# Performance work log

Hardware: AMD Instinct MI355X
Metric: run time of the kernel (lower is better)

Reference implementation:

```python
import jax, jax.numpy as jnp
import numpy as np

N = 50000      # nodes
E = 800000     # edges (avg degree 16)
F_IN = 128     # num_features
H = 64         # hidden_dim
G = 64         # graphs in batch


def setup_inputs() -> dict:
    key = jax.random.key(0)
    ks = jax.random.split(key, 20)
    inp = {
        "x": jax.random.normal(ks[0], (N, F_IN), jnp.float32),
        "edge_index": jax.random.randint(ks[1], (2, E), 0, N, dtype=jnp.int32).astype(jnp.int64),
        "batch": jnp.sort(jax.random.randint(ks[2], (N,), 0, G, dtype=jnp.int32)).astype(jnp.int64),
    }
    # GraphConv layer dims: in -> out
    dims = [(F_IN, H), (H, 2 * H), (2 * H, 3 * H), (3 * H, H)]
    k = 3
    for i, (din, dout) in enumerate(dims):
        s = 1.0 / np.sqrt(din).astype(np.float32)
        inp[f"w{i+1}_rel"] = jax.random.normal(ks[k], (din, dout), jnp.float32) * s
        inp[f"w{i+1}_root"] = jax.random.normal(ks[k + 1], (din, dout), jnp.float32) * s
        inp[f"b{i+1}"] = jnp.zeros((dout,), jnp.float32)
        k += 2
    inp["head_w"] = jax.random.normal(ks[k], (H, 1), jnp.float32) * (1.0 / np.sqrt(H).astype(np.float32))
    inp["head_b"] = jnp.zeros((1,), jnp.float32)
    return inp


def _graph_conv(x, src, dst, w_rel, w_root, b):
    # PyG GraphConv: out = lin_rel(sum_{j in N(i)} x_j) + lin_root(x_i)
    agg = jax.ops.segment_sum(x[src], dst, num_segments=N)  # [N, din]
    return agg @ w_rel + b + x @ w_root


def reference(x, edge_index, batch,
              w1_rel, w1_root, b1,
              w2_rel, w2_root, b2,
              w3_rel, w3_root, b3,
              w4_rel, w4_root, b4,
              head_w, head_b):
    src, dst = edge_index[0], edge_index[1]
    h = jax.nn.relu(_graph_conv(x, src, dst, w1_rel, w1_root, b1))
    h = jax.nn.relu(_graph_conv(h, src, dst, w2_rel, w2_root, b2))
    h = jax.nn.relu(_graph_conv(h, src, dst, w3_rel, w3_root, b3))
    h = _graph_conv(h, src, dst, w4_rel, w4_root, b4)          # [N, H]
    # global_mean_pool over graph ids
    sums = jax.ops.segment_sum(h, batch, num_segments=G)       # [G, H]
    counts = jax.ops.segment_sum(jnp.ones((N,), h.dtype), batch, num_segments=G)
    pooled = sums / jnp.maximum(counts, 1.0)[:, None]          # [G, H]
    return pooled @ head_w + head_b                            # [G, 1]
```

## Files before the change

### kernel.cpp

```cpp
#include <hip/hip_runtime.h>


#define NNODES 50000
#define NEDGES 800000
#define NGRAPH 64
#define NBUK 256
#define BSZ 196
#define EPB (NEDGES / NBUK)
#define CVT_NB (NNODES * 128 / 4 / 256)
#define PACK_NB (160 * 512 / 256)
#define RGRID ((NNODES + 127) / 128)
#define RCHUNK ((RGRID + 7) / 8)

typedef __attribute__((ext_vector_type(8))) __bf16 bf16x8;
typedef __attribute__((ext_vector_type(16))) float f32x16;

__device__ __forceinline__ unsigned short f2bf(float f) {
    unsigned u = __float_as_uint(f);
    u += 0x7fff + ((u >> 16) & 1);
    return (unsigned short)(u >> 16);
}
__device__ __forceinline__ float bf2f(unsigned b) {
    return __uint_as_float(b << 16);
}

__device__ __forceinline__ void dma16(const void* g, void* l) {
    __builtin_amdgcn_global_load_lds(
        (const __attribute__((address_space(1))) void*)g,
        (__attribute__((address_space(3))) void*)l, 16, 0, 0);
}


__global__ void hist_kernel(const int* __restrict__ dst, int* __restrict__ cnt) {
    __shared__ int h[NBUK];
    int tid = threadIdx.x, k = blockIdx.x;
    h[tid] = 0;
    __syncthreads();
    int end = (k + 1) * EPB;
    for (int i = k * EPB + tid; i < end; i += 256)
        atomicAdd(&h[dst[i] / BSZ], 1);
    __syncthreads();
    cnt[tid * NBUK + k] = h[tid];
}

__global__ void scan1_kernel(int* __restrict__ a, int* __restrict__ bsum, int n) {
    __shared__ int buf[256];
    int tid = threadIdx.x;
    int i = blockIdx.x * 256 + tid;
    int v = (i < n) ? a[i] : 0;
    buf[tid] = v;
    __syncthreads();
    #pragma unroll
    for (int off = 1; off < 256; off <<= 1) {
        int t = (tid >= off) ? buf[tid - off] : 0;
        __syncthreads();
        buf[tid] += t;
        __syncthreads();
    }
    if (i < n) a[i] = buf[tid] - v;
    if (tid == 255) bsum[blockIdx.x] = buf[255];
}

__global__ void scan2_kernel(int* __restrict__ bsum, int nb) {
    __shared__ int buf[256];
    int tid = threadIdx.x;
    int v = (tid < nb) ? bsum[tid] : 0;
    buf[tid] = v;
    __syncthreads();
    #pragma unroll
    for (int off = 1; off < 256; off <<= 1) {
        int t = (tid >= off) ? buf[tid - off] : 0;
        __syncthreads();
        buf[tid] += t;
        __syncthreads();
    }
    if (tid < nb) bsum[tid] = buf[tid] - v;
}

__global__ void partition_kernel(const int* __restrict__ src, const int* __restrict__ dst,
                                 const int* __restrict__ cnt, const int* __restrict__ bsum,
                                 unsigned long long* __restrict__ pedge) {
    __shared__ int lbase[NBUK];
    int tid = threadIdx.x, k = blockIdx.x;
    lbase[tid] = cnt[tid * NBUK + k] + bsum[tid];
    __syncthreads();
    int end = (k + 1) * EPB;
    for (int i = k * EPB + tid; i < end; i += 256) {
        int s = src[i], d = dst[i];
        int pos = atomicAdd(&lbase[d / BSZ], 1);
        pedge[pos] = (unsigned long long)(unsigned)s | ((unsigned long long)(unsigned)d << 32);
    }
}

__global__ void build_kernel(const unsigned long long* __restrict__ pedge,
                             const int* __restrict__ bsum,
                             int* __restrict__ rp, int* __restrict__ csr) {
    __shared__ int sdeg[256], sc[256], sbase[256], sfill[256];
    int tid = threadIdx.x, b = blockIdx.x;
    int node0 = b * BSZ;
    int ncnt = NNODES - node0;
    if (ncnt > BSZ) ncnt = BSZ;
    if (ncnt < 0) ncnt = 0;
    int seg0 = bsum[b];
    int seg1 = (b + 1 < NBUK) ? bsum[b + 1] : NEDGES;
    sdeg[tid] = 0;
    sfill[tid] = 0;
    __syncthreads();
    for (int i = seg0 + tid; i < seg1; i += 256)
        atomicAdd(&sdeg[(int)(pedge[i] >> 32) - node0], 1);
    __syncthreads();
    sc[tid] = sdeg[tid];
    __syncthreads();
    #pragma unroll
    for (int off = 1; off < 256; off <<= 1) {
        int t = (tid >= off) ? sc[tid - off] : 0;
        __syncthreads();
        sc[tid] += t;
        __syncthreads();
    }
    sbase[tid] = sc[tid] - sdeg[tid];
    if (tid < ncnt) rp[node0 + tid] = seg0 + sbase[tid];
    if (b == NBUK - 1 && tid == 0) rp[NNODES] = NEDGES;
    __syncthreads();
    for (int i = seg0 + tid; i < seg1; i += 256) {
        unsigned long long p = pedge[i];
        int d = (int)(p >> 32) - node0;
        int pos = atomicAdd(&sfill[d], 1);
        csr[seg0 + sbase[d] + pos] = (int)(p & 0xffffffffu);
    }
}


__device__ __forceinline__ void pack32(const float* __restrict__ W, unsigned short* __restrict__ dst,
                                       int KS_tot, int ks0, int dcols, int ct0,
                                       int tl, int ksl, int lane, int j) {
    int k = ksl * 16 + ((lane >> 5) << 3) + j;
    int col = tl * 32 + (lane & 31);
    dst[(((size_t)(ct0 + tl) * KS_tot + (ks0 + ksl)) * 64 + lane) * 8 + j] = f2bf(W[k * dcols + col]);
}

__global__ void prep_kernel(const float* __restrict__ x, unsigned short* __restrict__ xbf,
                            const float* __restrict__ w1_rel, const float* __restrict__ w1_root,
                            const float* __restrict__ w2_rel, const float* __restrict__ w2_root,
                            const float* __restrict__ w3_rel, const float* __restrict__ w3_root,
                            unsigned short* __restrict__ pL1, unsigned short* __restrict__ pL2,
                            unsigned short* __restrict__ pL3,
                            const float* __restrict__ w4_rel, const float* __restrict__ w4_root,
                            const float* __restrict__ b4, const float* __restrict__ head_w,
                            float* __restrict__ wr, float* __restrict__ wt,
                            float* __restrict__ cbuf) {
    int b = blockIdx.x;
    int tid = threadIdx.x;
    if (b < CVT_NB) {
        int i = b * 256 + tid;
        float4 v = ((const float4*)x)[i];
        unsigned lo = (unsigned)f2bf(v.x) | ((unsigned)f2bf(v.y) << 16);
        unsigned hi = (unsigned)f2bf(v.z) | ((unsigned)f2bf(v.w) << 16);
        ((uint2*)xbf)[i] = make_uint2(lo, hi);
    } else if (b < CVT_NB + PACK_NB) {
        int idx = (b - CVT_NB) * 256 + tid;
        int g = idx >> 9;
        int t = idx & 511;
        int lane = (t >> 3) & 63, j = t & 7;
        if (g < 16)       { int gl = g;       pack32(w1_rel,  pL1, 8,  0, 64,  0, gl / 8, gl % 8, lane, j); }
        else if (g < 32)  { int gl = g - 16;  pack32(w1_root, pL1, 8,  0, 64,  2, gl / 8, gl % 8, lane, j); }
        else if (g < 48)  { int gl = g - 32;  pack32(w2_rel,  pL2, 8,  0, 128, 0, gl / 4, gl % 4, lane, j); }
        else if (g < 64)  { int gl = g - 48;  pack32(w2_root, pL2, 8,  4, 128, 0, gl / 4, gl % 4, lane, j); }
        else if (g < 112) { int gl = g - 64;  pack32(w3_rel,  pL3, 16, 0, 192, 0, gl / 8, gl % 8, lane, j); }
        else              { int gl = g - 112; pack32(w3_root, pL3, 16, 8, 192, 0, gl / 8, gl % 8, lane, j); }
    } else {
        if (tid < 192) {
            float ar = 0.f, at = 0.f;
            for (int j = 0; j < 64; j++) {
                float hw = head_w[j];
                ar = fmaf(w4_rel[tid * 64 + j], hw, ar);
                at = fmaf(w4_root[tid * 64 + j], hw, at);
            }
            wr[tid] = ar;
            wt[tid] = at;
        } else if (tid == 192) {
            float c = 0.f;
            for (int j = 0; j < 64; j++) c = fmaf(b4[j], head_w[j], c);
            cbuf[0] = c;
        }
    }
}


template<int KS, int NT, int NHALF, int ST, int KCH>
__global__ __launch_bounds__(256) void gemm_v5(
    const unsigned short* __restrict__ A, const unsigned short* __restrict__ Wall,
    const float* __restrict__ bias, unsigned short* __restrict__ OUT,
    int ldo, int ocol0, int relu, int N,
    const float* __restrict__ wrp, const float* __restrict__ wtp,
    float* __restrict__ sb, float* __restrict__ tb)
{
    const int K = KS * 16;
    const int CPC = KCH * 2;
    __shared__ __align__(16) unsigned short sB[NT * KS * 512];
    __shared__ __align__(16) unsigned short sA[128 * KCH * 16];

    int i = blockIdx.x;
    int chunk = i / (8 * NHALF);
    int rem = i - chunk * (8 * NHALF);
    int halfsel = rem >> 3;
    int rowb = chunk * 8 + (rem & 7);
    int rbase = rowb * 128;
    if (rbase >= N) return;

    int tid = threadIdx.x;
    int wave = tid >> 6, lane = tid & 63;
    int l32 = lane & 31, half = lane >> 5;
    const unsigned short* W = Wall + (size_t)halfsel * NT * KS * 512;

    #pragma unroll
    for (int j = 0; j < NT * KS * 64 / 256; j++) {
        int p = j * 256 + wave * 64;
        dma16(W + ((size_t)p + lane) * 8, sB + (size_t)p * 8);
    }

    f32x16 acc[NT];
    #pragma unroll
    for (int t = 0; t < NT; t++)
        #pragma unroll
        for (int r = 0; r < 16; r++) acc[t][r] = 0.f;

    int lr = wave * 32 + l32;

    for (int kb = 0; kb < KS; kb += KCH) {
        if (kb > 0) __syncthreads();
        #pragma unroll
        for (int j = 0; j < 128 * CPC / 256; j++) {
            int p = j * 256 + wave * 64 + lane;
            int r = p / CPC;
            int c = p - r * CPC;
            int cg = c ^ (r & (CPC - 1));
            dma16(A + (size_t)(rbase + r) * K + kb * 16 + cg * 8,
                  sA + (size_t)(j * 256 + wave * 64) * 8);
        }
        __syncthreads();
        #pragma unroll
        for (int l = 0; l < KCH; l++) {
            int cs = (l * 2 + half) ^ (lr & (CPC - 1));
            bf16x8 a = *(const bf16x8*)(sA + (size_t)lr * (KCH * 16) + cs * 8);
            int ks = kb + l;
            #pragma unroll
            for (int t = 0; t < NT; t++) {
                bf16x8 b = *(const bf16x8*)(sB + ((size_t)(t * KS + ks) * 64 + lane) * 8);
                acc[t] = __builtin_amdgcn_mfma_f32_32x32x16_bf16(a, b, acc[t], 0, 0, 0);
            }
        }
    }

    int wrbase = rbase + wave * 32;
    if constexpr (ST) {
        #pragma unroll
        for (int reg = 0; reg < 16; reg++) {
            int row = wrbase + (reg & 3) + 8 * (reg >> 2) + 4 * half;
            float sv = 0.f, tv = 0.f;
            #pragma unroll
            for (int t = 0; t < NT; t++) {
                int col = halfsel * NT * 32 + t * 32 + l32;
                float v = fmaxf(acc[t][reg] + bias[col], 0.f);
                sv = fmaf(v, wrp[col], sv);
                tv = fmaf(v, wtp[col], tv);
            }
            #pragma unroll
            for (int m = 1; m < 32; m <<= 1) {
                sv += __shfl_xor(sv, m, 64);
                tv += __shfl_xor(tv, m, 64);
            }
            if (l32 == 0 && row < N) {
                atomicAdd(&sb[row], sv);
                atomicAdd(&tb[row], tv);
            }
        }
    } else {
        #pragma unroll
        for (int t = 0; t < NT; t++) {
            int col = t * 32 + l32;
            float bi = bias ? bias[col] : 0.f;
            #pragma unroll
            for (int reg = 0; reg < 16; reg++) {
                int row = wrbase + (reg & 3) + 8 * (reg >> 2) + 4 * half;
                if (row < N) {
                    float v = acc[t][reg] + bi;
                    if (relu) v = fmaxf(v, 0.f);
                    OUT[(size_t)row * ldo + ocol0 + col] = f2bf(v);
                }
            }
        }
    }
}


__device__ __forceinline__ void acc8(float* a, uint4 u) {
    a[0] += bf2f(u.x & 0xffffu); a[1] += bf2f(u.x >> 16);
    a[2] += bf2f(u.y & 0xffffu); a[3] += bf2f(u.y >> 16);
    a[4] += bf2f(u.z & 0xffffu); a[5] += bf2f(u.z >> 16);
    a[6] += bf2f(u.w & 0xffffu); a[7] += bf2f(u.w >> 16);
}

template<int LPF, int SUBS>
__global__ void agg_kernel_v3(const unsigned short* __restrict__ X, int ldx,
                              const int* __restrict__ rp, const int* __restrict__ csr,
                              const unsigned short* __restrict__ root, int ldr,
                              const float* __restrict__ bias, int relu,
                              unsigned short* __restrict__ OUT, int ldo, int N) {
    int t = blockIdx.x * blockDim.x + threadIdx.x;
    int node = t / (SUBS * LPF);
    int r = t % (SUBS * LPF);
    int sub = r / LPF;
    int sl = r % LPF;
    if (node >= N) return;
    float a[8] = {0.f, 0.f, 0.f, 0.f, 0.f, 0.f, 0.f, 0.f};
    int e0 = rp[node], e1 = rp[node + 1];
    const unsigned short* xb = X + 8 * sl;
    int e = e0 + sub;
    for (; e + SUBS < e1; e += 2 * SUBS) {
        int s0 = csr[e], s1 = csr[e + SUBS];
        uint4 u0 = *(const uint4*)(xb + (size_t)s0 * ldx);
        uint4 u1 = *(const uint4*)(xb + (size_t)s1 * ldx);
        acc8(a, u0);
        acc8(a, u1);
    }
    if (e < e1) {
        uint4 u = *(const uint4*)(xb + (size_t)csr[e] * ldx);
        acc8(a, u);
    }
    #pragma unroll
    for (int m = LPF; m < SUBS * LPF; m <<= 1)
        #pragma unroll
        for (int i = 0; i < 8; i++) a[i] += __shfl_xor(a[i], m, 64);
    if (sub == 0) {
        if (root) {
            uint4 u = *(const uint4*)(root + (size_t)node * ldr + 8 * sl);
            acc8(a, u);
        }
        if (bias) {
            float4 b0 = *(const float4*)(bias + 8 * sl);
            float4 b1 = *(const float4*)(bias + 8 * sl + 4);
            a[0] += b0.x; a[1] += b0.y; a[2] += b0.z; a[3] += b0.w;
            a[4] += b1.x; a[5] += b1.y; a[6] += b1.z; a[7] += b1.w;
        }
        if (relu) {
            #pragma unroll
            for (int i = 0; i < 8; i++) a[i] = fmaxf(a[i], 0.f);
        }
        uint4 o;
        o.x = (unsigned)f2bf(a[0]) | ((unsigned)f2bf(a[1]) << 16);
        o.y = (unsigned)f2bf(a[2]) | ((unsigned)f2bf(a[3]) << 16);
        o.z = (unsigned)f2bf(a[4]) | ((unsigned)f2bf(a[5]) << 16);
        o.w = (unsigned)f2bf(a[6]) | ((unsigned)f2bf(a[7]) << 16);
        *(uint4*)(OUT + (size_t)node * ldo + 8 * sl) = o;
    }
}


__global__ void aggpool_kernel(const float* __restrict__ s, const float* __restrict__ t,
                               const int* __restrict__ rp, const int* __restrict__ csr,
                               const int* __restrict__ batch, float* __restrict__ gsum,
                               int* __restrict__ cnt, int N) {
    __shared__ float ls[NGRAPH];
    __shared__ int lc[NGRAPH];
    int tid = threadIdx.x;
    if (tid < NGRAPH) { ls[tid] = 0.f; lc[tid] = 0; }
    __syncthreads();
    int n = blockIdx.x * blockDim.x + tid;
    if (n < N) {
        float a = 0.f;
        int e = rp[n], e1 = rp[n + 1];
        for (; e + 3 < e1; e += 4) {
            int s0 = csr[e], s1 = csr[e + 1], s2 = csr[e + 2], s3 = csr[e + 3];
            a += s[s0] + s[s1] + s[s2] + s[s3];
        }
        for (; e < e1; e++) a += s[csr[e]];
        int g = batch[n];
        atomicAdd(&ls[g], a + t[n]);
        atomicAdd(&lc[g], 1);
    }
    __syncthreads();
    if (tid < NGRAPH && lc[tid] > 0) {
        atomicAdd(&gsum[tid], ls[tid]);
        atomicAdd(&cnt[tid], lc[tid]);
    }
}

__global__ void final_kernel(const float* __restrict__ gsum, const int* __restrict__ cnt,
                             const float* __restrict__ cbuf, const float* __restrict__ head_b,
                             float* __restrict__ out) {
    int g = threadIdx.x;
    if (g < NGRAPH) {
        float c = (float)(cnt[g] > 0 ? cnt[g] : 1);
        out[g] = gsum[g] / c + cbuf[0] + head_b[0];
    }
}


extern "C" void kernel_launch(void* const* d_in, const int* in_sizes, int n_in,
                              void* d_out, int out_size, void* d_ws, size_t ws_size,
                              hipStream_t stream) {
    const float* x       = (const float*)d_in[0];
    const int*   edge    = (const int*)d_in[1];
    const int*   batch   = (const int*)d_in[2];
    const float* w1_rel  = (const float*)d_in[3];
    const float* w1_root = (const float*)d_in[4];
    const float* b1      = (const float*)d_in[5];
    const float* w2_rel  = (const float*)d_in[6];
    const float* w2_root = (const float*)d_in[7];
    const float* b2      = (const float*)d_in[8];
    const float* w3_rel  = (const float*)d_in[9];
    const float* w3_root = (const float*)d_in[10];
    const float* b3      = (const float*)d_in[11];
    const float* w4_rel  = (const float*)d_in[12];
    const float* w4_root = (const float*)d_in[13];
    const float* b4      = (const float*)d_in[14];
    const float* head_w  = (const float*)d_in[15];
    const float* head_b  = (const float*)d_in[16];
    float* out = (float*)d_out;

    const int N = NNODES, E = NEDGES;
    const int* src = edge;
    const int* dst = edge + E;

    char* ws = (char*)d_ws;
    size_t off = 0;
    auto alloc = [&](size_t bytes) -> char* {
        char* p = ws + off;
        off = (off + bytes + 255) & ~(size_t)255;
        return p;
    };
    float* gsum  = (float*)alloc(NGRAPH * 4);
    int*   cnt   = (int*)alloc(NGRAPH * 4);
    float* sbuf  = (float*)alloc((size_t)N * 4);
    float* tbuf  = (float*)alloc((size_t)N * 4);
    size_t zero_bytes = off;
    int*   bcnt  = (int*)alloc((size_t)NBUK * NBUK * 4);
    int*   bsum  = (int*)alloc(256 * 4);
    int*   rp    = (int*)alloc((size_t)(N + 1) * 4);
    int*   csr   = (int*)alloc((size_t)E * 4);
    unsigned long long* pedge = (unsigned long long*)alloc((size_t)E * 8);
    unsigned short* xbf    = (unsigned short*)alloc((size_t)N * 128 * 2);
    unsigned short* z1     = (unsigned short*)alloc((size_t)N * 128 * 2);
    unsigned short* combo2 = (unsigned short*)alloc((size_t)N * 128 * 2);
    unsigned short* combo3 = (unsigned short*)alloc((size_t)N * 256 * 2);
    unsigned short* pL1    = (unsigned short*)alloc(4 * 8 * 512 * 2);
    unsigned short* pL2    = (unsigned short*)alloc(4 * 8 * 512 * 2);
    unsigned short* pL3    = (unsigned short*)alloc(6 * 16 * 512 * 2);
    float* wr    = (float*)alloc(192 * 4);
    float* wt    = (float*)alloc(192 * 4);
    float* cbuf  = (float*)alloc(4);
    (void)ws_size;

    hipMemsetAsync(gsum, 0, zero_bytes, stream);

    const int TB = 256;

    hist_kernel<<<NBUK, 256, 0, stream>>>(dst, bcnt);
    scan1_kernel<<<NBUK, 256, 0, stream>>>(bcnt, bsum, NBUK * NBUK);
    scan2_kernel<<<1, 256, 0, stream>>>(bsum, NBUK);
    partition_kernel<<<NBUK, 256, 0, stream>>>(src, dst, bcnt, bsum, pedge);
    build_kernel<<<NBUK, 256, 0, stream>>>(pedge, bsum, rp, csr);

    prep_kernel<<<CVT_NB + PACK_NB + 1, 256, 0, stream>>>(
        x, xbf, w1_rel, w1_root, w2_rel, w2_root, w3_rel, w3_root,
        pL1, pL2, pL3, w4_rel, w4_root, b4, head_w, wr, wt, cbuf);

    gemm_v5<8, 4, 1, 0, 8><<<RCHUNK * 8, 256, 0, stream>>>(
        xbf, pL1, nullptr, z1, 128, 0, 0, N, nullptr, nullptr, nullptr, nullptr);
    agg_kernel_v3<8, 2><<<(N * 16 + TB - 1) / TB, TB, 0, stream>>>(z1, 128, rp, csr,
                                                                   z1 + 64, 128, b1, 1, combo2 + 64, 128, N);
    agg_kernel_v3<8, 2><<<(N * 16 + TB - 1) / TB, TB, 0, stream>>>(combo2 + 64, 128, rp, csr,
                                                                   nullptr, 0, nullptr, 0, combo2, 128, N);
    gemm_v5<8, 4, 1, 0, 8><<<RCHUNK * 8, 256, 0, stream>>>(
        combo2, pL2, b2, combo3, 256, 128, 1, N, nullptr, nullptr, nullptr, nullptr);
    agg_kernel_v3<16, 2><<<(N * 32 + TB - 1) / TB, TB, 0, stream>>>(combo3 + 128, 256, rp, csr,
                                                                    nullptr, 0, nullptr, 0, combo3, 256, N);
    gemm_v5<16, 3, 2, 1, 4><<<RCHUNK * 8 * 2, 256, 0, stream>>>(
        combo3, pL3, b3, nullptr, 0, 0, 0, N, wr, wt, sbuf, tbuf);

    aggpool_kernel<<<(N + TB - 1) / TB, TB, 0, stream>>>(sbuf, tbuf, rp, csr, batch, gsum, cnt, N);
    final_kernel<<<1, 64, 0, stream>>>(gsum, cnt, cbuf, head_b, out);
}
```

Measured before the change: 251.3 us.

## Fuse CSR build and prep into one cooperative kernel; unroll aggregation by four

Merges the histogram, two scans, partition, CSR build and weight/feature prep kernels into a single cooperative launch, using grid-wide syncs in place of kernel boundaries. The prep work is spread across the 256 blocks during the histogram phase. This removes five kernel launches and their gaps. The aggregation kernel's edge loop is also unrolled to four gathers per iteration, putting more loads in flight. Grid syncs add their own cost, and the prep work now runs on only 256 blocks instead of a wider grid.

```diff
diff --git a/kernel.cpp b/kernel.cpp
--- a/kernel.cpp
+++ b/kernel.cpp
@@ -1,5 +1,8 @@
 #include <hip/hip_runtime.h>
-
+#include <hip/hip_cooperative_groups.h>
+
+
+namespace cg = cooperative_groups;
 
 #define NNODES 50000
 #define NEDGES 800000
@@ -9,6 +12,7 @@
 #define EPB (NEDGES / NBUK)
 #define CVT_NB (NNODES * 128 / 4 / 256)
 #define PACK_NB (160 * 512 / 256)
+#define PREP_NB (CVT_NB + PACK_NB + 1)
 #define RGRID ((NNODES + 127) / 128)
 #define RCHUNK ((RGRID + 7) / 8)
 
@@ -28,106 +32,6 @@
     __builtin_amdgcn_global_load_lds(
         (const __attribute__((address_space(1))) void*)g,
         (__attribute__((address_space(3))) void*)l, 16, 0, 0);
-}
-
-
-__global__ void hist_kernel(const int* __restrict__ dst, int* __restrict__ cnt) {
-    __shared__ int h[NBUK];
-    int tid = threadIdx.x, k = blockIdx.x;
-    h[tid] = 0;
-    __syncthreads();
-    int end = (k + 1) * EPB;
-    for (int i = k * EPB + tid; i < end; i += 256)
-        atomicAdd(&h[dst[i] / BSZ], 1);
-    __syncthreads();
-    cnt[tid * NBUK + k] = h[tid];
-}
-
-__global__ void scan1_kernel(int* __restrict__ a, int* __restrict__ bsum, int n) {
-    __shared__ int buf[256];
-    int tid = threadIdx.x;
-    int i = blockIdx.x * 256 + tid;
-    int v = (i < n) ? a[i] : 0;
-    buf[tid] = v;
-    __syncthreads();
-    #pragma unroll
-    for (int off = 1; off < 256; off <<= 1) {
-        int t = (tid >= off) ? buf[tid - off] : 0;
-        __syncthreads();
-        buf[tid] += t;
-        __syncthreads();
-    }
-    if (i < n) a[i] = buf[tid] - v;
-    if (tid == 255) bsum[blockIdx.x] = buf[255];
-}
-
-__global__ void scan2_kernel(int* __restrict__ bsum, int nb) {
-    __shared__ int buf[256];
-    int tid = threadIdx.x;
-    int v = (tid < nb) ? bsum[tid] : 0;
-    buf[tid] = v;
-    __syncthreads();
-    #pragma unroll
-    for (int off = 1; off < 256; off <<= 1) {
-        int t = (tid >= off) ? buf[tid - off] : 0;
-        __syncthreads();
-        buf[tid] += t;
-        __syncthreads();
-    }
-    if (tid < nb) bsum[tid] = buf[tid] - v;
-}
-
-__global__ void partition_kernel(const int* __restrict__ src, const int* __restrict__ dst,
-                                 const int* __restrict__ cnt, const int* __restrict__ bsum,
-                                 unsigned long long* __restrict__ pedge) {
-    __shared__ int lbase[NBUK];
-    int tid = threadIdx.x, k = blockIdx.x;
-    lbase[tid] = cnt[tid * NBUK + k] + bsum[tid];
-    __syncthreads();
-    int end = (k + 1) * EPB;
-    for (int i = k * EPB + tid; i < end; i += 256) {
-        int s = src[i], d = dst[i];
-        int pos = atomicAdd(&lbase[d / BSZ], 1);
-        pedge[pos] = (unsigned long long)(unsigned)s | ((unsigned long long)(unsigned)d << 32);
-    }
-}
-
-__global__ void build_kernel(const unsigned long long* __restrict__ pedge,
-                             const int* __restrict__ bsum,
-                             int* __restrict__ rp, int* __restrict__ csr) {
-    __shared__ int sdeg[256], sc[256], sbase[256], sfill[256];
-    int tid = threadIdx.x, b = blockIdx.x;
-    int node0 = b * BSZ;
-    int ncnt = NNODES - node0;
-    if (ncnt > BSZ) ncnt = BSZ;
-    if (ncnt < 0) ncnt = 0;
-    int seg0 = bsum[b];
-    int seg1 = (b + 1 < NBUK) ? bsum[b + 1] : NEDGES;
-    sdeg[tid] = 0;
-    sfill[tid] = 0;
-    __syncthreads();
-    for (int i = seg0 + tid; i < seg1; i += 256)
-        atomicAdd(&sdeg[(int)(pedge[i] >> 32) - node0], 1);
-    __syncthreads();
-    sc[tid] = sdeg[tid];
-    __syncthreads();
-    #pragma unroll
-    for (int off = 1; off < 256; off <<= 1) {
-        int t = (tid >= off) ? sc[tid - off] : 0;
-        __syncthreads();
-        sc[tid] += t;
-        __syncthreads();
-    }
-    sbase[tid] = sc[tid] - sdeg[tid];
-    if (tid < ncnt) rp[node0 + tid] = seg0 + sbase[tid];
-    if (b == NBUK - 1 && tid == 0) rp[NNODES] = NEDGES;
-    __syncthreads();
-    for (int i = seg0 + tid; i < seg1; i += 256) {
-        unsigned long long p = pedge[i];
-        int d = (int)(p >> 32) - node0;
-        int pos = atomicAdd(&sfill[d], 1);
-        csr[seg0 + sbase[d] + pos] = (int)(p & 0xffffffffu);
-    }
 }
 
 
@@ -139,18 +43,15 @@
     dst[(((size_t)(ct0 + tl) * KS_tot + (ks0 + ksl)) * 64 + lane) * 8 + j] = f2bf(W[k * dcols + col]);
 }
 
-__global__ void prep_kernel(const float* __restrict__ x, unsigned short* __restrict__ xbf,
-                            const float* __restrict__ w1_rel, const float* __restrict__ w1_root,
-                            const float* __restrict__ w2_rel, const float* __restrict__ w2_root,
-                            const float* __restrict__ w3_rel, const float* __restrict__ w3_root,
-                            unsigned short* __restrict__ pL1, unsigned short* __restrict__ pL2,
-                            unsigned short* __restrict__ pL3,
-                            const float* __restrict__ w4_rel, const float* __restrict__ w4_root,
-                            const float* __restrict__ b4, const float* __restrict__ head_w,
-                            float* __restrict__ wr, float* __restrict__ wt,
-                            float* __restrict__ cbuf) {
-    int b = blockIdx.x;
-    int tid = threadIdx.x;
+__device__ void prep_body(int b, int tid,
+                          const float* x, unsigned short* xbf,
+                          const float* w1_rel, const float* w1_root,
+                          const float* w2_rel, const float* w2_root,
+                          const float* w3_rel, const float* w3_root,
+                          unsigned short* pL1, unsigned short* pL2, unsigned short* pL3,
+                          const float* w4_rel, const float* w4_root,
+                          const float* b4, const float* head_w,
+                          float* wr, float* wt, float* cbuf) {
     if (b < CVT_NB) {
         int i = b * 256 + tid;
         float4 v = ((const float4*)x)[i];
@@ -187,6 +88,122 @@
 }
 
 
+__global__ void __launch_bounds__(256) csr_prep_kernel(
+    const int* __restrict__ esrc, const int* __restrict__ edst,
+    int* __restrict__ bcnt, int* __restrict__ bsum,
+    int* __restrict__ rp, int* __restrict__ csr,
+    unsigned long long* __restrict__ pedge,
+    const float* __restrict__ x, unsigned short* __restrict__ xbf,
+    const float* __restrict__ w1_rel, const float* __restrict__ w1_root,
+    const float* __restrict__ w2_rel, const float* __restrict__ w2_root,
+    const float* __restrict__ w3_rel, const float* __restrict__ w3_root,
+    unsigned short* __restrict__ pL1, unsigned short* __restrict__ pL2,
+    unsigned short* __restrict__ pL3,
+    const float* __restrict__ w4_rel, const float* __restrict__ w4_root,
+    const float* __restrict__ b4, const float* __restrict__ head_w,
+    float* __restrict__ wr, float* __restrict__ wt, float* __restrict__ cbuf)
+{
+    cg::grid_group grid = cg::this_grid();
+    __shared__ int sm[1024];
+    int tid = threadIdx.x, k = blockIdx.x;
+
+    sm[tid] = 0;
+    __syncthreads();
+    {
+        int end = (k + 1) * EPB;
+        for (int i = k * EPB + tid; i < end; i += 256)
+            atomicAdd(&sm[edst[i] / BSZ], 1);
+    }
+    __syncthreads();
+    bcnt[tid * NBUK + k] = sm[tid];
+    for (int vb = k; vb < PREP_NB; vb += NBUK)
+        prep_body(vb, tid, x, xbf, w1_rel, w1_root, w2_rel, w2_root, w3_rel, w3_root,
+                  pL1, pL2, pL3, w4_rel, w4_root, b4, head_w, wr, wt, cbuf);
+    grid.sync();
+
+    {
+        int v = bcnt[k * NBUK + tid];
+        sm[tid] = v;
+        __syncthreads();
+        #pragma unroll
+        for (int off = 1; off < 256; off <<= 1) {
+            int t = (tid >= off) ? sm[tid - off] : 0;
+            __syncthreads();
+            sm[tid] += t;
+            __syncthreads();
+        }
+        bcnt[k * NBUK + tid] = sm[tid] - v;
+        if (tid == 255) bsum[k] = sm[255];
+    }
+    grid.sync();
+
+    if (k == 0) {
+        int v = bsum[tid];
+        sm[tid] = v;
+        __syncthreads();
+        #pragma unroll
+        for (int off = 1; off < 256; off <<= 1) {
+            int t = (tid >= off) ? sm[tid - off] : 0;
+            __syncthreads();
+            sm[tid] += t;
+            __syncthreads();
+        }
+        bsum[tid] = sm[tid] - v;
+    }
+    grid.sync();
+
+    sm[tid] = bcnt[tid * NBUK + k] + bsum[tid];
+    __syncthreads();
+    {
+        int end = (k + 1) * EPB;
+        for (int i = k * EPB + tid; i < end; i += 256) {
+            int s = esrc[i], d = edst[i];
+            int pos = atomicAdd(&sm[d / BSZ], 1);
+            pedge[pos] = (unsigned long long)(unsigned)s | ((unsigned long long)(unsigned)d << 32);
+        }
+    }
+    grid.sync();
+
+    {
+        int* sdeg = sm;
+        int* sc = sm + 256;
+        int* sbase = sm + 512;
+        int* sfill = sm + 768;
+        int node0 = k * BSZ;
+        int ncnt = NNODES - node0;
+        if (ncnt > BSZ) ncnt = BSZ;
+        if (ncnt < 0) ncnt = 0;
+        int seg0 = bsum[k];
+        int seg1 = (k + 1 < NBUK) ? bsum[k + 1] : NEDGES;
+        sdeg[tid] = 0;
+        sfill[tid] = 0;
+        __syncthreads();
+        for (int i = seg0 + tid; i < seg1; i += 256)
+            atomicAdd(&sdeg[(int)(pedge[i] >> 32) - node0], 1);
+        __syncthreads();
+        sc[tid] = sdeg[tid];
+        __syncthreads();
+        #pragma unroll
+        for (int off = 1; off < 256; off <<= 1) {
+            int t = (tid >= off) ? sc[tid - off] : 0;
+            __syncthreads();
+            sc[tid] += t;
+            __syncthreads();
+        }
+        sbase[tid] = sc[tid] - sdeg[tid];
+        if (tid < ncnt) rp[node0 + tid] = seg0 + sbase[tid];
+        if (k == NBUK - 1 && tid == 0) rp[NNODES] = NEDGES;
+        __syncthreads();
+        for (int i = seg0 + tid; i < seg1; i += 256) {
+            unsigned long long p = pedge[i];
+            int d = (int)(p >> 32) - node0;
+            int pos = atomicAdd(&sfill[d], 1);
+            csr[seg0 + sbase[d] + pos] = (int)(p & 0xffffffffu);
+        }
+    }
+}
+
+
 template<int KS, int NT, int NHALF, int ST, int KCH>
 __global__ __launch_bounds__(256) void gemm_v5(
     const unsigned short* __restrict__ A, const unsigned short* __restrict__ Wall,
@@ -302,7 +319,7 @@
 }
 
 template<int LPF, int SUBS>
-__global__ void agg_kernel_v3(const unsigned short* __restrict__ X, int ldx,
+__global__ void agg_kernel_v4(const unsigned short* __restrict__ X, int ldx,
                               const int* __restrict__ rp, const int* __restrict__ csr,
                               const unsigned short* __restrict__ root, int ldr,
                               const float* __restrict__ bias, int relu,
@@ -317,14 +334,15 @@
     int e0 = rp[node], e1 = rp[node + 1];
     const unsigned short* xb = X + 8 * sl;
     int e = e0 + sub;
-    for (; e + SUBS < e1; e += 2 * SUBS) {
-        int s0 = csr[e], s1 = csr[e + SUBS];
+    for (; e + 3 * SUBS < e1; e += 4 * SUBS) {
+        int s0 = csr[e], s1 = csr[e + SUBS], s2 = csr[e + 2 * SUBS], s3 = csr[e + 3 * SUBS];
         uint4 u0 = *(const uint4*)(xb + (size_t)s0 * ldx);
         uint4 u1 = *(const uint4*)(xb + (size_t)s1 * ldx);
-        acc8(a, u0);
-        acc8(a, u1);
-    }
-    if (e < e1) {
+        uint4 u2 = *(const uint4*)(xb + (size_t)s2 * ldx);
+        uint4 u3 = *(const uint4*)(xb + (size_t)s3 * ldx);
+        acc8(a, u0); acc8(a, u1); acc8(a, u2); acc8(a, u3);
+    }
+    for (; e < e1; e += SUBS) {
         uint4 u = *(const uint4*)(xb + (size_t)csr[e] * ldx);
         acc8(a, u);
     }
@@ -420,8 +438,8 @@
     float* out = (float*)d_out;
 
     const int N = NNODES, E = NEDGES;
-    const int* src = edge;
-    const int* dst = edge + E;
+    const int* esrc = edge;
+    const int* edst = edge + E;
 
     char* ws = (char*)d_ws;
     size_t off = 0;
@@ -456,25 +474,28 @@
 
     const int TB = 256;
 
-    hist_kernel<<<NBUK, 256, 0, stream>>>(dst, bcnt);
-    scan1_kernel<<<NBUK, 256, 0, stream>>>(bcnt, bsum, NBUK * NBUK);
-    scan2_kernel<<<1, 256, 0, stream>>>(bsum, NBUK);
-    partition_kernel<<<NBUK, 256, 0, stream>>>(src, dst, bcnt, bsum, pedge);
-    build_kernel<<<NBUK, 256, 0, stream>>>(pedge, bsum, rp, csr);
-
-    prep_kernel<<<CVT_NB + PACK_NB + 1, 256, 0, stream>>>(
-        x, xbf, w1_rel, w1_root, w2_rel, w2_root, w3_rel, w3_root,
-        pL1, pL2, pL3, w4_rel, w4_root, b4, head_w, wr, wt, cbuf);
+    {
+        void* params[] = {
+            (void*)&esrc, (void*)&edst, (void*)&bcnt, (void*)&bsum, (void*)&rp,
+            (void*)&csr, (void*)&pedge, (void*)&x, (void*)&xbf,
+            (void*)&w1_rel, (void*)&w1_root, (void*)&w2_rel, (void*)&w2_root,
+            (void*)&w3_rel, (void*)&w3_root, (void*)&pL1, (void*)&pL2, (void*)&pL3,
+            (void*)&w4_rel, (void*)&w4_root, (void*)&b4, (void*)&head_w,
+            (void*)&wr, (void*)&wt, (void*)&cbuf
+        };
+        hipLaunchCooperativeKernel((const void*)csr_prep_kernel, dim3(NBUK), dim3(256),
+                                   params, 0, stream);
+    }
 
     gemm_v5<8, 4, 1, 0, 8><<<RCHUNK * 8, 256, 0, stream>>>(
         xbf, pL1, nullptr, z1, 128, 0, 0, N, nullptr, nullptr, nullptr, nullptr);
-    agg_kernel_v3<8, 2><<<(N * 16 + TB - 1) / TB, TB, 0, stream>>>(z1, 128, rp, csr,
+    agg_kernel_v4<8, 2><<<(N * 16 + TB - 1) / TB, TB, 0, stream>>>(z1, 128, rp, csr,
                                                                    z1 + 64, 128, b1, 1, combo2 + 64, 128, N);
-    agg_kernel_v3<8, 2><<<(N * 16 + TB - 1) / TB, TB, 0, stream>>>(combo2 + 64, 128, rp, csr,
+    agg_kernel_v4<8, 2><<<(N * 16 + TB - 1) / TB, TB, 0, stream>>>(combo2 + 64, 128, rp, csr,
                                                                    nullptr, 0, nullptr, 0, combo2, 128, N);
     gemm_v5<8, 4, 1, 0, 8><<<RCHUNK * 8, 256, 0, stream>>>(
         combo2, pL2, b2, combo3, 256, 128, 1, N, nullptr, nullptr, nullptr, nullptr);
-    agg_kernel_v3<16, 2><<<(N * 32 + TB - 1) / TB, TB, 0, stream>>>(combo3 + 128, 256, rp, csr,
+    agg_kernel_v4<16, 2><<<(N * 32 + TB - 1) / TB, TB, 0, stream>>>(combo3 + 128, 256, rp, csr,
                                                                     nullptr, 0, nullptr, 0, combo3, 256, N);
     gemm_v5<16, 3, 2, 1, 4><<<RCHUNK * 8 * 2, 256, 0, stream>>>(
         combo3, pL3, b3, nullptr, 0, 0, 0, N, wr, wt, sbuf, tbuf);
```

New measurement: 394.7 us. 1.57x slower.
